# Kernel tuning notes

Hardware: AMD Instinct MI355X
Metric: run time of the kernel (lower is better)

## Reference

```python
import jax, jax.numpy as jnp
import numpy as np
from jax import lax


def _leaky(x):
    # LeakyReLU, negative_slope=0.1
    return jnp.where(x > 0, x, 0.1 * x)


def _conv(x, w, pad, groups=1):
    # NCHW / OIHW 2D conv, stride 1
    return lax.conv_general_dilated(
        x, w, (1, 1), [(pad, pad), (pad, pad)],
        dimension_numbers=("NCHW", "OIHW", "NCHW"),
        feature_group_count=groups)


def setup_inputs() -> dict:
    key = jax.random.key(0)
    ks = jax.random.split(key, 12)
    B, C, H, W = 16, 64, 256, 256
    KS = 3

    def nrm(k, shape, fan_in):
        return jax.random.normal(k, shape, jnp.float32) / np.float32(np.sqrt(fan_in))

    return {
        "x": jax.random.normal(ks[0], (B, C, H, W), jnp.float32),
        "t": jax.random.normal(ks[1], (B, 1, 1, 1), jnp.float32),
        # t_process: 1x1 convs (1->64, 64->64), no bias -> stored as matrices
        "tW1": nrm(ks[2], (C, 1), 1),
        "tW2": nrm(ks[3], (C, C), C),
        # f_process: two 3x3 convs 64->64 with bias
        "fW1": nrm(ks[4], (C, C, KS, KS), C * KS * KS),
        "fb1": jnp.zeros((C,), jnp.float32),
        "fW2": nrm(ks[5], (C, C, KS, KS), C * KS * KS),
        "fb2": jnp.zeros((C,), jnp.float32),
        # kernel branch: 1x1 convs (1->64, 64->64*9), no bias
        "kW1": nrm(ks[6], (C, 1), 1),
        "kW2": nrm(ks[7], (C * KS * KS, C), C),
        # conv33: 3x3 conv 64->64 with bias
        "cW": nrm(ks[8], (C, C, KS, KS), C * KS * KS),
        "cb": jnp.zeros((C,), jnp.float32),
    }


def reference(x, t, tW1, tW2, fW1, fb1, fW2, fb2, kW1, kW2, cW, cb):
    b, c, h, w = x.shape
    KS = 3

    # f_process: Conv3x3 -> LeakyReLU -> Conv3x3 -> LeakyReLU
    f = _leaky(_conv(x, fW1, 1) + fb1[None, :, None, None])
    f = _leaky(_conv(f, fW2, 1) + fb2[None, :, None, None])

    # t is (b,1,1,1); 1x1 convs on it are per-sample matmuls
    ts = t.reshape(b, 1)
    # t_process: Conv1x1 -> LeakyReLU -> Conv1x1 -> Sigmoid -> (b,c,1,1)
    mv = jax.nn.sigmoid(_leaky(ts @ tW1.T) @ tW2.T).reshape(b, c, 1, 1)

    # kernel branch: Conv1x1 -> LeakyReLU -> Conv1x1 -> LeakyReLU -> (b*c,1,3,3)
    kern = _leaky(_leaky(ts @ kW1.T) @ kW2.T).reshape(b * c, 1, KS, KS)

    # per-sample-channel dynamic depthwise conv: groups = b*c
    out = _conv(f.reshape(1, b * c, h, w), kern, (KS - 1) // 2,
                groups=b * c).reshape(b, c, h, w)

    # modulation gating + residual 3x3 conv
    return out * mv + _conv(x, cW, 1) + cb[None, :, None, None]
```

## Files before the change

kernel.cpp:

```cpp
#include <hip/hip_runtime.h>
#include <cstdint>

using short8  = __attribute__((ext_vector_type(8))) short;
using short4v = __attribute__((ext_vector_type(4))) short;
using f32x16  = __attribute__((ext_vector_type(16))) float;
using float4v = __attribute__((ext_vector_type(4))) float;
typedef unsigned short ushort_t;

#define CHUNK_ROW 520
#define CHUNK_SLOTS 1560
#define BUF_SLOTS 1632
#define XSHW (BUF_SLOTS * 8)
#define WSHW (20 * 512)
#define XB0 WSHW
#define XB1 (WSHW + XSHW)
#define DYN_LDS ((WSHW + 2 * XSHW) * 2)

__device__ __forceinline__ float lrelu(float x) { return x > 0.f ? x : 0.1f * x; }

__device__ __forceinline__ ushort_t f2bf(float f) {
    union { float f; unsigned u; } v; v.f = f;
    unsigned r = (v.u + 0x7FFFu + ((v.u >> 16) & 1u)) >> 16;
    return (ushort_t)r;
}
__device__ __forceinline__ float bf2f(ushort_t b) {
    union { unsigned u; float f; } v; v.u = ((unsigned)b) << 16; return v.f;
}

__device__ __forceinline__ void gload_lds16(const ushort_t* g, ushort_t* l) {
    __builtin_amdgcn_global_load_lds(
        (const __attribute__((address_space(1))) void*)g,
        (__attribute__((address_space(3))) void*)l, 16, 0, 0);
}

#define VMCNT(n) asm volatile("s_waitcnt vmcnt(" #n ")" ::: "memory")
#define RBAR() __builtin_amdgcn_s_barrier()
#define SCHED0() __builtin_amdgcn_sched_barrier(0)

__global__ void k_tiny(const float* __restrict__ t, const float* __restrict__ tW1,
                       const float* __restrict__ tW2, const float* __restrict__ kW1,
                       const float* __restrict__ kW2, float* __restrict__ ktr) {
    int b = blockIdx.x;
    int c = threadIdx.x;
    __shared__ float h1[64], g1[64];
    float ts = t[b];
    h1[c] = lrelu(ts * tW1[c]);
    g1[c] = lrelu(ts * kW1[c]);
    __syncthreads();
    float s = 0.f;
    for (int j = 0; j < 64; ++j) s = fmaf(tW2[c * 64 + j], h1[j], s);
    float mvv = 1.f / (1.f + expf(-s));
    for (int q = 0; q < 9; ++q) {
        float s2 = 0.f;
        for (int j = 0; j < 64; ++j) s2 = fmaf(kW2[(c * 9 + q) * 64 + j], g1[j], s2);
        ktr[b * 576 + q * 64 + c] = lrelu(s2) * mvv;
    }
}

__global__ void k_zrow(ushort_t* __restrict__ z) {
    int i = blockIdx.x * 256 + threadIdx.x;
    *(short8*)(z + (size_t)i * 8) = (short8)0;
}

__global__ void k_pack(const float* __restrict__ w1, const float* __restrict__ w2,
                       const float* __restrict__ w3, ushort_t* __restrict__ wp) {
    int idx = blockIdx.x * 256 + threadIdx.x;
    if (idx >= 3 * 36864) return;
    int conv = idx / 36864, r = idx % 36864;
    const float* W = conv == 0 ? w1 : (conv == 1 ? w2 : w3);
    int j = r & 7, lane = (r >> 3) & 63;
    int rr = r >> 9;
    int chunk = rr / 18, row = rr % 18;
    int t = row >> 1, ct = row & 1;
    int co = ct * 32 + (lane & 31);
    int ci = chunk * 16 + (lane >> 5) * 8 + j;
    wp[idx] = f2bf(W[(co * 64 + ci) * 9 + t]);
}

__global__ __launch_bounds__(256) void k_tr(const float* __restrict__ x,
                                            ushort_t* __restrict__ xbf) {
    int bid = blockIdx.x;
    int h = bid & 255, b = bid >> 8;
    int t = threadIdx.x;
    for (int it = 0; it < 8; ++it) {
        int idx = t + it * 256;
        int g = idx & 7, w = idx >> 3;
        const float* src = x + (((size_t)(b * 64 + g * 8) * 256 + h) * 256 + w);
        short8 v;
#pragma unroll
        for (int j = 0; j < 8; ++j) v[j] = (short)f2bf(src[(size_t)j * 65536]);
        *(short8*)(xbf + (((size_t)(b * 256 + h) * 256 + w) * 64 + g * 8)) = v;
    }
}

#define STAGE_X(chunk, xbase)                                                    \
    {                                                                            \
        _Pragma("unroll")                                                        \
        for (int i_ = 0; i_ < 7; ++i_) {                                         \
            int base_ = wv * 390 + i_ * 64;                                      \
            int S_ = base_ + lane;                                               \
            S_ = S_ < CHUNK_SLOTS ? S_ : CHUNK_SLOTS - 1;                        \
            int row_ = (S_ >= 2 * CHUNK_ROW) ? 2 : (S_ >= CHUNK_ROW ? 1 : 0);    \
            int rem_ = S_ - row_ * CHUNK_ROW;                                    \
            int mg_ = rem_ >> 3, sl_ = rem_ & 7;                                 \
            int sp_ = sl_ ^ (mg_ & 7);                                           \
            int p_ = mg_ * 4 + (sp_ >> 1), g_ = sp_ & 1;                         \
            int wsx_ = p_ - 1;                                                   \
            bool edge_ = (unsigned)wsx_ >= 256u;                                 \
            const ushort_t* rp_ = (row_ == 0) ? rb0 : (row_ == 1 ? rb1 : rb2);   \
            const ushort_t* src_ =                                               \
                edge_ ? zv : (rp_ + wsx_ * 64 + (chunk)*16 + g_ * 8);            \
            gload_lds16(src_, xs + (xbase) + (size_t)base_ * 8);                 \
        }                                                                        \
    }

#define STAGE_W(chunk)                                                           \
    {                                                                            \
        _Pragma("unroll")                                                        \
        for (int i_ = 0; i_ < 5; ++i_) {                                         \
            int row_ = wv * 5 + i_;                                              \
            int rc_ = row_ > 17 ? 17 : row_;                                     \
            gload_lds16(wp + (size_t)((chunk)*18 + rc_) * 512 + lane * 8,        \
                        xs + (size_t)row_ * 512);                                \
        }                                                                        \
    }

#define COMPUTE(xbase)                                                           \
    {                                                                            \
        __builtin_amdgcn_s_setprio(1);                                           \
        _Pragma("unroll")                                                        \
        for (int t_ = 0; t_ < 9; ++t_) {                                         \
            short8 a0 = *(const short8*)(xs + (size_t)(t_ * 2) * 512 + lane * 8);\
            short8 a1 = *(const short8*)(xs + (size_t)(t_ * 2 + 1) * 512 + lane * 8); \
            const int dwx_ = t_ % 3, rr_ = t_ / 3;                               \
            _Pragma("unroll")                                                    \
            for (int pt_ = 0; pt_ < 2; ++pt_) {                                  \
                int p_ = pw0 + pt_ * 32 + l31 + dwx_;                            \
                int mg_ = p_ >> 2;                                               \
                int sl_ = ((p_ & 3) * 2 + lhi) ^ (mg_ & 7);                      \
                short8 bf = *(const short8*)(                                    \
                    xs + (xbase) + (size_t)(rr_ * CHUNK_ROW + mg_ * 8 + sl_) * 8);\
                acc[0][pt_] = __builtin_amdgcn_mfma_f32_32x32x16_bf16(           \
                    a0, bf, acc[0][pt_], 0, 0, 0);                               \
                acc[1][pt_] = __builtin_amdgcn_mfma_f32_32x32x16_bf16(           \
                    a1, bf, acc[1][pt_], 0, 0, 0);                               \
            }                                                                    \
        }                                                                        \
        __builtin_amdgcn_s_setprio(0);                                           \
    }

template <int OMODE>
__global__ __launch_bounds__(256, 2) void k_conv(
    const ushort_t* __restrict__ in, const ushort_t* __restrict__ zv,
    const ushort_t* __restrict__ wp, const float* __restrict__ bias,
    void* __restrict__ outp) {
    extern __shared__ __align__(16) ushort_t xs[];
    const int tid = threadIdx.x;
    const int lane = tid & 63;
    const int wv = tid >> 6;
    const unsigned bid = blockIdx.x;
    const unsigned L = (bid & 7u) * 512u + (bid >> 3);
    const int h = L & 255, b = L >> 8;
    const int l31 = lane & 31, lhi = lane >> 5;
    const int pw0 = wv * 64;

    const ushort_t* rb0 = (h > 0)   ? in + ((size_t)(b * 256 + h - 1)) * 16384 : zv;
    const ushort_t* rb1 =             in + ((size_t)(b * 256 + h)) * 16384;
    const ushort_t* rb2 = (h < 255) ? in + ((size_t)(b * 256 + h + 1)) * 16384 : zv;

    f32x16 acc[2][2];
#pragma unroll
    for (int a = 0; a < 2; ++a)
#pragma unroll
        for (int c = 0; c < 2; ++c) acc[a][c] = (f32x16)0.0f;

    STAGE_W(0);
    STAGE_X(0, XB0);
    STAGE_X(1, XB1);
    VMCNT(7);
    RBAR(); SCHED0();
    COMPUTE(XB0);
    RBAR();
    STAGE_W(1); STAGE_X(2, XB0);
    VMCNT(7);
    RBAR(); SCHED0();
    COMPUTE(XB1);
    RBAR();
    STAGE_W(2); STAGE_X(3, XB1);
    VMCNT(7);
    RBAR(); SCHED0();
    COMPUTE(XB0);
    RBAR();
    STAGE_W(3);
    VMCNT(0);
    RBAR(); SCHED0();
    COMPUTE(XB1);

    const int co_b = 4 * lhi;
    if (OMODE == 0) {
        ushort_t* outb = (ushort_t*)outp + ((size_t)(b * 256 + h)) * 16384;
#pragma unroll
        for (int ct = 0; ct < 2; ++ct)
#pragma unroll
            for (int pt = 0; pt < 2; ++pt) {
                int pix = pw0 + pt * 32 + l31;
                ushort_t* po = outb + (size_t)pix * 64 + ct * 32 + co_b;
#pragma unroll
                for (int q = 0; q < 4; ++q) {
                    float4v bv = *(const float4v*)(bias + ct * 32 + co_b + 8 * q);
                    short4v sv;
#pragma unroll
                    for (int m = 0; m < 4; ++m) {
                        float v = lrelu(acc[ct][pt][q * 4 + m] + bv[m]);
                        sv[m] = (short)f2bf(v);
                    }
                    *(short4v*)(po + 8 * q) = sv;
                }
            }
    } else if (OMODE == 1) {
        ushort_t* pb = (ushort_t*)outp + (((size_t)b * 64) << 16) + h * 256;
#pragma unroll
        for (int ct = 0; ct < 2; ++ct)
#pragma unroll
            for (int pt = 0; pt < 2; ++pt) {
                int pix = pw0 + pt * 32 + l31;
#pragma unroll
                for (int q = 0; q < 4; ++q) {
                    float4v bv = *(const float4v*)(bias + ct * 32 + co_b + 8 * q);
#pragma unroll
                    for (int m = 0; m < 4; ++m) {
                        int c = ct * 32 + co_b + 8 * q + m;
                        float v = lrelu(acc[ct][pt][q * 4 + m] + bv[m]);
                        pb[((size_t)c << 16) + pix] = f2bf(v);
                    }
                }
            }
    } else {
        float* pb = (float*)outp + (((size_t)b * 64) << 16) + h * 256;
#pragma unroll
        for (int ct = 0; ct < 2; ++ct)
#pragma unroll
            for (int pt = 0; pt < 2; ++pt) {
                int pix = pw0 + pt * 32 + l31;
#pragma unroll
                for (int q = 0; q < 4; ++q) {
                    float4v bv = *(const float4v*)(bias + ct * 32 + co_b + 8 * q);
#pragma unroll
                    for (int m = 0; m < 4; ++m) {
                        int c = ct * 32 + co_b + 8 * q + m;
                        pb[((size_t)c << 16) + pix] = acc[ct][pt][q * 4 + m] + bv[m];
                    }
                }
            }
    }
}

__global__ __launch_bounds__(256) void k_fin(const ushort_t* __restrict__ f2,
                                             const float* __restrict__ ktr,
                                             float* __restrict__ out) {
    __shared__ __align__(16) ushort_t s[10 * 272];
    const unsigned bid = blockIdx.x;
    const unsigned L = (bid & 7u) * 4096u + (bid >> 3);
    const int hb = L & 31, c = (L >> 5) & 63, b = L >> 11;
    const int h0 = hb * 8;
    const int w = threadIdx.x;

    const ushort_t* f2c = f2 + (((size_t)(b * 64 + c)) << 16);
    for (int i = w; i < 320; i += 256) {
        int r = i >> 5, seg = i & 31;
        int hs = h0 - 1 + r;
        short8 v = (short8)0;
        if ((unsigned)hs < 256u) v = *(const short8*)(f2c + hs * 256 + seg * 8);
        *(short8*)(&s[r * 272 + 8 + seg * 8]) = v;
        if (seg == 0) s[r * 272 + 7] = 0;
        if (seg == 31) s[r * 272 + 264] = 0;
    }
    __syncthreads();

    float kv[9];
#pragma unroll
    for (int t9 = 0; t9 < 9; ++t9) kv[t9] = ktr[b * 576 + t9 * 64 + c];

    float lv[10], cv[10], rv[10];
#pragma unroll
    for (int r = 0; r < 10; ++r) {
        lv[r] = bf2f(s[r * 272 + 7 + w]);
        cv[r] = bf2f(s[r * 272 + 8 + w]);
        rv[r] = bf2f(s[r * 272 + 9 + w]);
    }

    float* ob = out + (((size_t)(b * 64 + c)) << 16) + h0 * 256 + w;
#pragma unroll
    for (int rr = 0; rr < 8; ++rr) {
        float dwv = 0.f;
#pragma unroll
        for (int r3 = 0; r3 < 3; ++r3) {
            dwv = fmaf(kv[r3 * 3 + 0], lv[rr + r3], dwv);
            dwv = fmaf(kv[r3 * 3 + 1], cv[rr + r3], dwv);
            dwv = fmaf(kv[r3 * 3 + 2], rv[rr + r3], dwv);
        }
        float* po = ob + rr * 256;
        *po = *po + dwv;
    }
}

extern "C" void kernel_launch(void* const* d_in, const int* in_sizes, int n_in,
                              void* d_out, int out_size, void* d_ws, size_t ws_size,
                              hipStream_t stream) {
    const float* x   = (const float*)d_in[0];
    const float* t   = (const float*)d_in[1];
    const float* tW1 = (const float*)d_in[2];
    const float* tW2 = (const float*)d_in[3];
    const float* fW1 = (const float*)d_in[4];
    const float* fb1 = (const float*)d_in[5];
    const float* fW2 = (const float*)d_in[6];
    const float* fb2 = (const float*)d_in[7];
    const float* kW1 = (const float*)d_in[8];
    const float* kW2 = (const float*)d_in[9];
    const float* cW  = (const float*)d_in[10];
    const float* cb  = (const float*)d_in[11];

    char* ws = (char*)d_ws;
    float*    ktr  = (float*)ws;
    ushort_t* wp   = (ushort_t*)(ws + 65536);
    ushort_t* zv   = (ushort_t*)(ws + 294912);
    ushort_t* xbf  = (ushort_t*)(ws + (512u << 10));
    ushort_t* f2n  = (ushort_t*)(ws + (512u << 10) + ((size_t)128 << 20));
    ushort_t* f1bf = (ushort_t*)d_out;
    float*    out  = (float*)d_out;

    hipFuncSetAttribute(reinterpret_cast<const void*>(&k_conv<0>),
                        hipFuncAttributeMaxDynamicSharedMemorySize, DYN_LDS);
    hipFuncSetAttribute(reinterpret_cast<const void*>(&k_conv<1>),
                        hipFuncAttributeMaxDynamicSharedMemorySize, DYN_LDS);
    hipFuncSetAttribute(reinterpret_cast<const void*>(&k_conv<2>),
                        hipFuncAttributeMaxDynamicSharedMemorySize, DYN_LDS);

    k_tiny<<<dim3(16), dim3(64), 0, stream>>>(t, tW1, tW2, kW1, kW2, ktr);
    k_zrow<<<dim3(8), dim3(256), 0, stream>>>(zv);
    k_pack<<<dim3((3 * 36864 + 255) / 256), dim3(256), 0, stream>>>(fW1, fW2, cW, wp);
    k_tr<<<dim3(4096), dim3(256), 0, stream>>>(x, xbf);

    k_conv<0><<<dim3(4096), dim3(256), DYN_LDS, stream>>>(xbf, zv, wp, fb1, (void*)f1bf);
    k_conv<1><<<dim3(4096), dim3(256), DYN_LDS, stream>>>(f1bf, zv, wp + 36864, fb2, (void*)f2n);
    k_conv<2><<<dim3(4096), dim3(256), DYN_LDS, stream>>>(xbf, zv, wp + 2 * 36864, cb, (void*)out);
    k_fin<<<dim3(32768), dim3(256), 0, stream>>>(f2n, ktr, out);
}
```

Measured before the change: 609.8 us.

## Fuse first f_process conv and residual conv into one kernel sharing input tiles

Both 3x3 convolutions that read x (fW1 and cW) now run in a single kernel, k_conv02. It stages each input chunk into LDS once and issues MFMAs against two weight sets, which removes one full pass over the bf16 input and one kernel launch. The fused kernel is single-buffered with no double-buffer overlap and holds twice the accumulators, so it risks register spills or lower occupancy. Workspace buffers are also reassigned: f2 now reuses the xbf buffer, and f1 moves into the workspace instead of the output buffer.

Result: faster. 586.7 us (-3.8%).

```diff
diff --git a/kernel.cpp b/kernel.cpp
--- a/kernel.cpp
+++ b/kernel.cpp
@@ -14,7 +14,10 @@
 #define WSHW (20 * 512)
 #define XB0 WSHW
 #define XB1 (WSHW + XSHW)
-#define DYN_LDS ((WSHW + 2 * XSHW) * 2)
+#define DYN1 ((WSHW + 2 * XSHW) * 2)
+#define WSHM (40 * 512)
+#define XBM WSHM
+#define DYN02 ((WSHM + XSHW) * 2)
 
 __device__ __forceinline__ float lrelu(float x) { return x > 0.f ? x : 0.1f * x; }
 
@@ -63,18 +66,36 @@
 }
 
 __global__ void k_pack(const float* __restrict__ w1, const float* __restrict__ w2,
-                       const float* __restrict__ w3, ushort_t* __restrict__ wp) {
+                       const float* __restrict__ w3, ushort_t* __restrict__ wpM,
+                       ushort_t* __restrict__ wp2) {
     int idx = blockIdx.x * 256 + threadIdx.x;
-    if (idx >= 3 * 36864) return;
-    int conv = idx / 36864, r = idx % 36864;
-    const float* W = conv == 0 ? w1 : (conv == 1 ? w2 : w3);
-    int j = r & 7, lane = (r >> 3) & 63;
-    int rr = r >> 9;
-    int chunk = rr / 18, row = rr % 18;
+    const int NM = 4 * 36 * 512;
+    if (idx >= NM + 4 * 18 * 512) return;
+    const float* W;
+    ushort_t* dst;
+    int chunk, row, e;
+    if (idx < NM) {
+        chunk = idx / (36 * 512);
+        int rem = idx % (36 * 512);
+        row = rem / 512;
+        e = rem % 512;
+        W = (row < 18) ? w1 : w3;
+        dst = wpM + idx;
+        row %= 18;
+    } else {
+        int i2 = idx - NM;
+        chunk = i2 / (18 * 512);
+        int rem = i2 % (18 * 512);
+        row = rem / 512;
+        e = rem % 512;
+        W = w2;
+        dst = wp2 + i2;
+    }
+    int lane = e >> 3, j = e & 7;
     int t = row >> 1, ct = row & 1;
     int co = ct * 32 + (lane & 31);
     int ci = chunk * 16 + (lane >> 5) * 8 + j;
-    wp[idx] = f2bf(W[(co * 64 + ci) * 9 + t]);
+    *dst = f2bf(W[(co * 64 + ci) * 9 + t]);
 }
 
 __global__ __launch_bounds__(256) void k_tr(const float* __restrict__ x,
@@ -121,6 +142,17 @@
             int row_ = wv * 5 + i_;                                              \
             int rc_ = row_ > 17 ? 17 : row_;                                     \
             gload_lds16(wp + (size_t)((chunk)*18 + rc_) * 512 + lane * 8,        \
+                        xs + (size_t)row_ * 512);                                \
+        }                                                                        \
+    }
+
+#define STAGE_WM(chunk)                                                          \
+    {                                                                            \
+        _Pragma("unroll")                                                        \
+        for (int i_ = 0; i_ < 10; ++i_) {                                        \
+            int row_ = wv * 10 + i_;                                             \
+            int rc_ = row_ > 35 ? 35 : row_;                                     \
+            gload_lds16(wpM + (size_t)((chunk)*36 + rc_) * 512 + lane * 8,       \
                         xs + (size_t)row_ * 512);                                \
         }                                                                        \
     }
@@ -149,11 +181,117 @@
         __builtin_amdgcn_s_setprio(0);                                           \
     }
 
-template <int OMODE>
-__global__ __launch_bounds__(256, 2) void k_conv(
+#define COMPUTE_M()                                                              \
+    {                                                                            \
+        __builtin_amdgcn_s_setprio(1);                                           \
+        _Pragma("unroll")                                                        \
+        for (int t_ = 0; t_ < 9; ++t_) {                                         \
+            short8 a0 = *(const short8*)(xs + (size_t)(t_ * 2) * 512 + lane * 8);\
+            short8 a1 = *(const short8*)(xs + (size_t)(t_ * 2 + 1) * 512 + lane * 8); \
+            short8 c0 = *(const short8*)(xs + (size_t)(18 + t_ * 2) * 512 + lane * 8); \
+            short8 c1 = *(const short8*)(xs + (size_t)(19 + t_ * 2) * 512 + lane * 8); \
+            const int dwx_ = t_ % 3, rr_ = t_ / 3;                               \
+            _Pragma("unroll")                                                    \
+            for (int pt_ = 0; pt_ < 2; ++pt_) {                                  \
+                int p_ = pw0 + pt_ * 32 + l31 + dwx_;                            \
+                int mg_ = p_ >> 2;                                               \
+                int sl_ = ((p_ & 3) * 2 + lhi) ^ (mg_ & 7);                      \
+                short8 bf = *(const short8*)(                                    \
+                    xs + XBM + (size_t)(rr_ * CHUNK_ROW + mg_ * 8 + sl_) * 8);   \
+                accA[0][pt_] = __builtin_amdgcn_mfma_f32_32x32x16_bf16(          \
+                    a0, bf, accA[0][pt_], 0, 0, 0);                              \
+                accA[1][pt_] = __builtin_amdgcn_mfma_f32_32x32x16_bf16(          \
+                    a1, bf, accA[1][pt_], 0, 0, 0);                              \
+                accC[0][pt_] = __builtin_amdgcn_mfma_f32_32x32x16_bf16(          \
+                    c0, bf, accC[0][pt_], 0, 0, 0);                              \
+                accC[1][pt_] = __builtin_amdgcn_mfma_f32_32x32x16_bf16(          \
+                    c1, bf, accC[1][pt_], 0, 0, 0);                              \
+            }                                                                    \
+        }                                                                        \
+        __builtin_amdgcn_s_setprio(0);                                           \
+    }
+
+__global__ __launch_bounds__(256, 2) void k_conv02(
+    const ushort_t* __restrict__ in, const ushort_t* __restrict__ zv,
+    const ushort_t* __restrict__ wpM, const float* __restrict__ ba,
+    const float* __restrict__ bc, ushort_t* __restrict__ f1out,
+    float* __restrict__ cres) {
+    extern __shared__ __align__(16) ushort_t xs[];
+    const int tid = threadIdx.x;
+    const int lane = tid & 63;
+    const int wv = tid >> 6;
+    const unsigned bid = blockIdx.x;
+    const unsigned L = (bid & 7u) * 512u + (bid >> 3);
+    const int h = L & 255, b = L >> 8;
+    const int l31 = lane & 31, lhi = lane >> 5;
+    const int pw0 = wv * 64;
+
+    const ushort_t* rb0 = (h > 0)   ? in + ((size_t)(b * 256 + h - 1)) * 16384 : zv;
+    const ushort_t* rb1 =             in + ((size_t)(b * 256 + h)) * 16384;
+    const ushort_t* rb2 = (h < 255) ? in + ((size_t)(b * 256 + h + 1)) * 16384 : zv;
+
+    f32x16 accA[2][2], accC[2][2];
+#pragma unroll
+    for (int a = 0; a < 2; ++a)
+#pragma unroll
+        for (int c = 0; c < 2; ++c) { accA[a][c] = (f32x16)0.0f; accC[a][c] = (f32x16)0.0f; }
+
+#pragma unroll
+    for (int ch = 0; ch < 4; ++ch) {
+        STAGE_WM(ch);
+        STAGE_X(ch, XBM);
+        VMCNT(0);
+        RBAR(); SCHED0();
+        COMPUTE_M();
+        RBAR();
+    }
+
+    const int co_b = 4 * lhi;
+    {
+        ushort_t* outb = f1out + ((size_t)(b * 256 + h)) * 16384;
+#pragma unroll
+        for (int ct = 0; ct < 2; ++ct)
+#pragma unroll
+            for (int pt = 0; pt < 2; ++pt) {
+                int pix = pw0 + pt * 32 + l31;
+                ushort_t* po = outb + (size_t)pix * 64 + ct * 32 + co_b;
+#pragma unroll
+                for (int q = 0; q < 4; ++q) {
+                    float4v bv = *(const float4v*)(ba + ct * 32 + co_b + 8 * q);
+                    short4v sv;
+#pragma unroll
+                    for (int m = 0; m < 4; ++m) {
+                        float v = lrelu(accA[ct][pt][q * 4 + m] + bv[m]);
+                        sv[m] = (short)f2bf(v);
+                    }
+                    *(short4v*)(po + 8 * q) = sv;
+                }
+            }
+    }
+    {
+        float* pb = cres + (((size_t)b * 64) << 16) + h * 256;
+#pragma unroll
+        for (int ct = 0; ct < 2; ++ct)
+#pragma unroll
+            for (int pt = 0; pt < 2; ++pt) {
+                int pix = pw0 + pt * 32 + l31;
+#pragma unroll
+                for (int q = 0; q < 4; ++q) {
+                    float4v bv = *(const float4v*)(bc + ct * 32 + co_b + 8 * q);
+#pragma unroll
+                    for (int m = 0; m < 4; ++m) {
+                        int c = ct * 32 + co_b + 8 * q + m;
+                        pb[((size_t)c << 16) + pix] = accC[ct][pt][q * 4 + m] + bv[m];
+                    }
+                }
+            }
+    }
+}
+
+__global__ __launch_bounds__(256, 2) void k_conv1(
     const ushort_t* __restrict__ in, const ushort_t* __restrict__ zv,
     const ushort_t* __restrict__ wp, const float* __restrict__ bias,
-    void* __restrict__ outp) {
+    ushort_t* __restrict__ outp) {
     extern __shared__ __align__(16) ushort_t xs[];
     const int tid = threadIdx.x;
     const int lane = tid & 63;
@@ -197,62 +335,23 @@
     COMPUTE(XB1);
 
     const int co_b = 4 * lhi;
-    if (OMODE == 0) {
-        ushort_t* outb = (ushort_t*)outp + ((size_t)(b * 256 + h)) * 16384;
-#pragma unroll
-        for (int ct = 0; ct < 2; ++ct)
-#pragma unroll
-            for (int pt = 0; pt < 2; ++pt) {
-                int pix = pw0 + pt * 32 + l31;
-                ushort_t* po = outb + (size_t)pix * 64 + ct * 32 + co_b;
-#pragma unroll
-                for (int q = 0; q < 4; ++q) {
-                    float4v bv = *(const float4v*)(bias + ct * 32 + co_b + 8 * q);
-                    short4v sv;
-#pragma unroll
-                    for (int m = 0; m < 4; ++m) {
-                        float v = lrelu(acc[ct][pt][q * 4 + m] + bv[m]);
-                        sv[m] = (short)f2bf(v);
-                    }
-                    *(short4v*)(po + 8 * q) = sv;
+    ushort_t* pb = outp + (((size_t)b * 64) << 16) + h * 256;
+#pragma unroll
+    for (int ct = 0; ct < 2; ++ct)
+#pragma unroll
+        for (int pt = 0; pt < 2; ++pt) {
+            int pix = pw0 + pt * 32 + l31;
+#pragma unroll
+            for (int q = 0; q < 4; ++q) {
+                float4v bv = *(const float4v*)(bias + ct * 32 + co_b + 8 * q);
+#pragma unroll
+                for (int m = 0; m < 4; ++m) {
+                    int c = ct * 32 + co_b + 8 * q + m;
+                    float v = lrelu(acc[ct][pt][q * 4 + m] + bv[m]);
+                    pb[((size_t)c << 16) + pix] = f2bf(v);
                 }
             }
-    } else if (OMODE == 1) {
-        ushort_t* pb = (ushort_t*)outp + (((size_t)b * 64) << 16) + h * 256;
-#pragma unroll
-        for (int ct = 0; ct < 2; ++ct)
-#pragma unroll
-            for (int pt = 0; pt < 2; ++pt) {
-                int pix = pw0 + pt * 32 + l31;
-#pragma unroll
-                for (int q = 0; q < 4; ++q) {
-                    float4v bv = *(const float4v*)(bias + ct * 32 + co_b + 8 * q);
-#pragma unroll
-                    for (int m = 0; m < 4; ++m) {
-                        int c = ct * 32 + co_b + 8 * q + m;
-                        float v = lrelu(acc[ct][pt][q * 4 + m] + bv[m]);
-                        pb[((size_t)c << 16) + pix] = f2bf(v);
-                    }
-                }
-            }
-    } else {
-        float* pb = (float*)outp + (((size_t)b * 64) << 16) + h * 256;
-#pragma unroll
-        for (int ct = 0; ct < 2; ++ct)
-#pragma unroll
-            for (int pt = 0; pt < 2; ++pt) {
-                int pix = pw0 + pt * 32 + l31;
-#pragma unroll
-                for (int q = 0; q < 4; ++q) {
-                    float4v bv = *(const float4v*)(bias + ct * 32 + co_b + 8 * q);
-#pragma unroll
-                    for (int m = 0; m < 4; ++m) {
-                        int c = ct * 32 + co_b + 8 * q + m;
-                        pb[((size_t)c << 16) + pix] = acc[ct][pt][q * 4 + m] + bv[m];
-                    }
-                }
-            }
-    }
+        }
 }
 
 __global__ __launch_bounds__(256) void k_fin(const ushort_t* __restrict__ f2,
@@ -322,27 +421,27 @@
 
     char* ws = (char*)d_ws;
     float*    ktr  = (float*)ws;
-    ushort_t* wp   = (ushort_t*)(ws + 65536);
+    ushort_t* wpM  = (ushort_t*)(ws + 65536);
+    ushort_t* wp2  = wpM + 4 * 36 * 512;
     ushort_t* zv   = (ushort_t*)(ws + 294912);
     ushort_t* xbf  = (ushort_t*)(ws + (512u << 10));
-    ushort_t* f2n  = (ushort_t*)(ws + (512u << 10) + ((size_t)128 << 20));
-    ushort_t* f1bf = (ushort_t*)d_out;
+    ushort_t* f1bf = (ushort_t*)(ws + (512u << 10) + ((size_t)128 << 20));
+    ushort_t* f2n  = xbf;
     float*    out  = (float*)d_out;
 
-    hipFuncSetAttribute(reinterpret_cast<const void*>(&k_conv<0>),
-                        hipFuncAttributeMaxDynamicSharedMemorySize, DYN_LDS);
-    hipFuncSetAttribute(reinterpret_cast<const void*>(&k_conv<1>),
-                        hipFuncAttributeMaxDynamicSharedMemorySize, DYN_LDS);
-    hipFuncSetAttribute(reinterpret_cast<const void*>(&k_conv<2>),
-                        hipFuncAttributeMaxDynamicSharedMemorySize, DYN_LDS);
+    hipFuncSetAttribute(reinterpret_cast<const void*>(&k_conv02),
+                        hipFuncAttributeMaxDynamicSharedMemorySize, DYN02);
+    hipFuncSetAttribute(reinterpret_cast<const void*>(&k_conv1),
+                        hipFuncAttributeMaxDynamicSharedMemorySize, DYN1);
 
     k_tiny<<<dim3(16), dim3(64), 0, stream>>>(t, tW1, tW2, kW1, kW2, ktr);
     k_zrow<<<dim3(8), dim3(256), 0, stream>>>(zv);
-    k_pack<<<dim3((3 * 36864 + 255) / 256), dim3(256), 0, stream>>>(fW1, fW2, cW, wp);
+    k_pack<<<dim3((4 * 36 * 512 + 4 * 18 * 512 + 255) / 256), dim3(256), 0, stream>>>(
+        fW1, fW2, cW, wpM, wp2);
     k_tr<<<dim3(4096), dim3(256), 0, stream>>>(x, xbf);
 
-    k_conv<0><<<dim3(4096), dim3(256), DYN_LDS, stream>>>(xbf, zv, wp, fb1, (void*)f1bf);
-    k_conv<1><<<dim3(4096), dim3(256), DYN_LDS, stream>>>(f1bf, zv, wp + 36864, fb2, (void*)f2n);
-    k_conv<2><<<dim3(4096), dim3(256), DYN_LDS, stream>>>(xbf, zv, wp + 2 * 36864, cb, (void*)out);
+    k_conv02<<<dim3(4096), dim3(256), DYN02, stream>>>(
+        xbf, zv, wpM, fb1, cb, f1bf, out);
+    k_conv1<<<dim3(4096), dim3(256), DYN1, stream>>>(f1bf, zv, wp2, fb2, f2n);
     k_fin<<<dim3(32768), dim3(256), 0, stream>>>(f2n, ktr, out);
 }
```
